# Kernel tuning notes

Hardware: AMD Instinct MI355X
Metric: run time of the kernel (lower is better)

## Reference

```python
import jax, jax.numpy as jnp
import numpy as np

N_NODES = 100000
N_EDGES = 1600000
IN_CH = 256
HID_CH = 32
OUT_CH = 8
N_GRAPHS = 64


def gcn_conv(x, edge_index, W, b):
    # PyG GCNConv: linear transform, add self-loops, symmetric norm, scatter-add.
    xw = x @ W  # [N, C_out]
    src, dst = edge_index[0], edge_index[1]
    loop = jnp.arange(N_NODES, dtype=src.dtype)
    src_f = jnp.concatenate([src, loop])  # [E+N]
    dst_f = jnp.concatenate([dst, loop])
    # degree over targets including self-loops (edge weight 1)
    deg = jax.ops.segment_sum(jnp.ones_like(dst_f, dtype=xw.dtype), dst_f,
                              num_segments=N_NODES)
    dinv = jnp.where(deg > 0, jax.lax.rsqrt(deg), 0.0)
    norm = dinv[src_f] * dinv[dst_f]  # [E+N]
    msgs = xw[src_f] * norm[:, None]  # gather + scale
    out = jax.ops.segment_sum(msgs, dst_f, num_segments=N_NODES)
    return out + b


def setup_inputs() -> dict:
    key = jax.random.key(0)
    k1, k2, k3, k4, k5, k6 = jax.random.split(key, 6)
    x = jax.random.normal(k1, (N_NODES, IN_CH), dtype=jnp.float32)
    edge_index = jax.random.randint(k2, (2, N_EDGES), 0, N_NODES, dtype=jnp.int64)
    batch = jnp.sort(jax.random.randint(k3, (N_NODES,), 0, N_GRAPHS, dtype=jnp.int64))
    s1 = 1.0 / np.sqrt(IN_CH)
    s2 = 1.0 / np.sqrt(HID_CH)
    W1 = jax.random.uniform(k4, (IN_CH, HID_CH), jnp.float32, -s1, s1)
    b1 = jnp.zeros((HID_CH,), jnp.float32)
    W2 = jax.random.uniform(k5, (HID_CH, OUT_CH), jnp.float32, -s2, s2)
    b2 = jnp.zeros((OUT_CH,), jnp.float32)
    return {"x": x, "edge_index": edge_index, "batch": batch,
            "W1": W1, "b1": b1, "W2": W2, "b2": b2}


def reference(x, edge_index, batch, W1, b1, W2, b2):
    h = jax.nn.relu(gcn_conv(x, edge_index, W1, b1))   # [N, HID]
    h = jax.nn.relu(gcn_conv(h, edge_index, W2, b2))   # [N, OUT]
    # global mean pool per graph
    sums = jax.ops.segment_sum(h, batch, num_segments=N_GRAPHS)
    cnts = jax.ops.segment_sum(jnp.ones((h.shape[0],), h.dtype), batch,
                               num_segments=N_GRAPHS)
    pooled = sums / jnp.maximum(cnts, 1.0)[:, None]    # [G, OUT]
    return jax.nn.log_softmax(pooled, axis=1)
```

## Files before the change

### kernel.cpp

```cpp
#include <hip/hip_runtime.h>
#include <hip/hip_bf16.h>
#include <math.h>

#define N_NODES 100000
#define N_EDGES 1600000
#define IN_CH 256
#define HID_CH 32
#define OUT_CH 8
#define N_GRAPHS 64

#define BUCK_SHIFT 7
#define NODES_PER_BUCK 128
#define NBUCK ((N_NODES + NODES_PER_BUCK - 1) / NODES_PER_BUCK)
#define CAP 2560
#define PCAP 3456
#define CHUNK 2048
#define NBLK_P1 ((N_EDGES + CHUNK - 1) / CHUNK)
#define ARENA (NBUCK * CAP)

#define DUMMY_ROW N_NODES
#define Y_ROWS 100008

#define OFF_DEG    0
#define OFF_DINV   (OFF_DEG + N_NODES)
#define OFF_ROWS   (OFF_DINV + N_NODES)
#define OFF_CNTG   (OFF_ROWS + N_NODES)
#define OFF_CSR    (OFF_CNTG + 784)
#define OFF_Y1     (OFF_CSR + NBUCK*PCAP)
#define OFF_BBUF   (OFF_Y1 + Y_ROWS*16)
#define OFF_Y2     (OFF_BBUF + ARENA)
#define OFF_PSUM   (OFF_Y2 + Y_ROWS*4)
#define OFF_PCNT   (OFF_PSUM + N_GRAPHS*OUT_CH)
#define OFF_WFRAG  (OFF_PCNT + 128)

typedef __attribute__((ext_vector_type(8))) short bf16x8;
typedef __attribute__((ext_vector_type(4))) float f32x4;

__device__ __forceinline__ unsigned bfr(float f) {
    unsigned u = __float_as_uint(f);
    return (u + 0x7fffu + ((u >> 16) & 1u)) >> 16;
}
__device__ __forceinline__ float bf_lo(unsigned w) { return __uint_as_float(w << 16); }
__device__ __forceinline__ float bf_hi(unsigned w) { return __uint_as_float(w & 0xffff0000u); }

#define ACC8(r) do { \
    a0 += bf_lo((r).x); a1 += bf_hi((r).x); a2 += bf_lo((r).y); a3 += bf_hi((r).y); \
    a4 += bf_lo((r).z); a5 += bf_hi((r).z); a6 += bf_lo((r).w); a7 += bf_hi((r).w); } while (0)

__global__ __launch_bounds__(256) void wprep_kernel(
        const float* __restrict__ W1, uint4* __restrict__ wfrag,
        unsigned* __restrict__ cntg, unsigned* __restrict__ y1w,
        unsigned* __restrict__ y2w) {
    const int t = threadIdx.x;
    if (blockIdx.x == 0) {
        for (int i = t; i < NBUCK; i += 256) cntg[i] = 0u;
        if (t < 16) y1w[(size_t)DUMMY_ROW * 16 + t] = 0u;
        if (t < 4)  y2w[(size_t)DUMMY_ROW * 4 + t] = 0u;
    }
    const int fl = blockIdx.x * 256 + t;
    const int f = fl >> 6, lane = fl & 63;
    const int kb = f >> 1, cb = f & 1;
    const int lr = lane & 15, lg = lane >> 4;
    unsigned short s[8];
#pragma unroll
    for (int j = 0; j < 8; j++)
        s[j] = (unsigned short)bfr(W1[(kb * 32 + lg * 8 + j) * 32 + cb * 16 + lr]);
    uint4 pk;
    pk.x = s[0] | ((unsigned)s[1] << 16);
    pk.y = s[2] | ((unsigned)s[3] << 16);
    pk.z = s[4] | ((unsigned)s[5] << 16);
    pk.w = s[6] | ((unsigned)s[7] << 16);
    wfrag[fl] = pk;
}

__global__ __launch_bounds__(256) void p1_partition(
        const int* __restrict__ src, const int* __restrict__ dst,
        unsigned* __restrict__ cntg, unsigned* __restrict__ bbuf) {
    __shared__ unsigned hcnt[NBUCK];
    __shared__ unsigned hcur[NBUCK];
    const int t = threadIdx.x;
    const long long e0 = (long long)blockIdx.x * CHUNK;

    int rs[8]; unsigned rd[8];
#pragma unroll
    for (int i = 0; i < 8; i++) {
        const long long e = e0 + t + i * 256;
        const bool v = (e < N_EDGES);
        rs[i] = v ? src[e] : 0;
        rd[i] = v ? (unsigned)dst[e] : 0xFFFFFFFFu;
    }
    for (int i = t; i < NBUCK; i += 256) hcnt[i] = 0;
    __syncthreads();
#pragma unroll
    for (int i = 0; i < 8; i++)
        if (rd[i] != 0xFFFFFFFFu) atomicAdd(&hcnt[rd[i] >> BUCK_SHIFT], 1u);
    __syncthreads();
    for (int i = t; i < NBUCK; i += 256) {
        const unsigned c = hcnt[i];
        const unsigned r = c ? atomicAdd(&cntg[i], c) : 0u;
        hcur[i] = (unsigned)i * CAP + r;
    }
    __syncthreads();
#pragma unroll
    for (int i = 0; i < 8; i++) {
        if (rd[i] != 0xFFFFFFFFu) {
            const unsigned b = rd[i] >> BUCK_SHIFT;
            const unsigned pos = atomicAdd(&hcur[b], 1u);
            if (pos - b * CAP < CAP)
                bbuf[pos] = (unsigned)rs[i] | ((rd[i] & (NODES_PER_BUCK - 1)) << 17);
        }
    }
}

__global__ __launch_bounds__(256) void p2_build(
        const unsigned* __restrict__ cntg,
        const unsigned* __restrict__ bbuf, int* __restrict__ csr,
        unsigned* __restrict__ deg, unsigned* __restrict__ rowstart,
        float* __restrict__ dinv) {
    __shared__ unsigned hist[NODES_PER_BUCK];
    __shared__ unsigned start[NODES_PER_BUCK];
    __shared__ unsigned cur[NODES_PER_BUCK];
    __shared__ unsigned s[256];
    __shared__ int lcsr[PCAP];
    const int b = blockIdx.x;
    const int t = threadIdx.x;
    unsigned cnt = cntg[b]; if (cnt > CAP) cnt = CAP;
    const unsigned* mybuf = bbuf + (size_t)b * CAP;

    if (t < NODES_PER_BUCK) hist[t] = 0;
    __syncthreads();
    for (unsigned i = t; i < cnt; i += 256) atomicAdd(&hist[mybuf[i] >> 17], 1u);
    __syncthreads();
    const unsigned d = (t < NODES_PER_BUCK) ? hist[t] : 0u;
    const unsigned pd = (d + 7u) & ~7u;
    s[t] = pd;
    __syncthreads();
    for (int off = 1; off < 256; off <<= 1) {
        unsigned x = (t >= off) ? s[t - off] : 0u;
        __syncthreads();
        s[t] += x;
        __syncthreads();
    }
    const unsigned total = s[255];
    const unsigned ex = s[t] - pd;
    if (t < NODES_PER_BUCK) { start[t] = ex; cur[t] = ex; }
    __syncthreads();
    for (unsigned i = t; i < total; i += 256) lcsr[i] = DUMMY_ROW;
    __syncthreads();
    for (unsigned i = t; i < cnt; i += 256) {
        const unsigned p = mybuf[i];
        const unsigned pos = atomicAdd(&cur[p >> 17], 1u);
        lcsr[pos] = (int)(p & 0x1FFFFu);
    }
    __syncthreads();
    const unsigned gbase = (unsigned)b * PCAP;
    for (unsigned i = t; i < total; i += 256) csr[gbase + i] = lcsr[i];
    const int n = b * NODES_PER_BUCK + t;
    if (t < NODES_PER_BUCK && n < N_NODES) {
        deg[n] = d;
        rowstart[n] = gbase + start[t];
        dinv[n] = rsqrtf((float)d + 1.0f);
    }
}

__global__ __launch_bounds__(256) void gemm1_kernel(
        const float* __restrict__ x, const uint4* __restrict__ wfrag,
        const float* __restrict__ dinv, unsigned short* __restrict__ y1bf,
        float* __restrict__ psum) {
    const int t = threadIdx.x;
    if (blockIdx.x == 0) {
        for (int i = t; i < N_GRAPHS * OUT_CH + N_GRAPHS; i += 256) psum[i] = 0.0f;
    }
    const int w = t >> 6;
    const int lane = t & 63;
    const int tile = blockIdx.x * 4 + w;
    if (tile >= N_NODES / 16) return;
    const int node0 = tile * 16;
    const int lr = lane & 15;
    const int lg = lane >> 4;

    bf16x8 bw[8][2];
#pragma unroll
    for (int kb = 0; kb < 8; kb++) {
#pragma unroll
        for (int cb = 0; cb < 2; cb++) {
            const uint4 v = wfrag[(kb * 2 + cb) * 64 + lane];
            bw[kb][cb] = *(const bf16x8*)&v;
        }
    }

    const float4* xr = (const float4*)(x + (size_t)(node0 + lr) * IN_CH);
    f32x4 acc0 = {0.f, 0.f, 0.f, 0.f}, acc1 = {0.f, 0.f, 0.f, 0.f};
#pragma unroll
    for (int kb = 0; kb < 8; kb++) {
        const float4 A = xr[kb * 8 + lg * 2];
        const float4 B = xr[kb * 8 + lg * 2 + 1];
        bf16x8 a;
        a[0] = (short)bfr(A.x); a[1] = (short)bfr(A.y);
        a[2] = (short)bfr(A.z); a[3] = (short)bfr(A.w);
        a[4] = (short)bfr(B.x); a[5] = (short)bfr(B.y);
        a[6] = (short)bfr(B.z); a[7] = (short)bfr(B.w);
        acc0 = __builtin_amdgcn_mfma_f32_16x16x32_bf16(a, bw[kb][0], acc0, 0, 0, 0);
        acc1 = __builtin_amdgcn_mfma_f32_16x16x32_bf16(a, bw[kb][1], acc1, 0, 0, 0);
    }

#pragma unroll
    for (int r = 0; r < 4; r++) {
        const int n = node0 + lg * 4 + r;
        const float dv = dinv[n];
        y1bf[(size_t)n * 32 + lr]      = (unsigned short)bfr(acc0[r] * dv);
        y1bf[(size_t)n * 32 + 16 + lr] = (unsigned short)bfr(acc1[r] * dv);
    }
}

__global__ __launch_bounds__(256) void g32l2_kernel(
        const unsigned* __restrict__ rowstart, const unsigned* __restrict__ deg,
        const int* __restrict__ csr, const uint4* __restrict__ y1v4,
        const float* __restrict__ dinv, const float* __restrict__ b1,
        const float* __restrict__ W2, uint4* __restrict__ y2v4) {
    __shared__ float w2s[HID_CH][9];
    __shared__ float b1s[HID_CH];
    const int t = threadIdx.x;
    { const int k = t >> 3, c = t & 7; w2s[k][c] = W2[t]; }
    if (t < HID_CH) b1s[t] = b1[t];
    __syncthreads();

    const int nl = t >> 2;
    const int q = t & 3;
    const int node = blockIdx.x * 64 + nl;
    if (node >= N_NODES) return;
    const int b4 = (t & 63) & ~3;

    const unsigned d = deg[node];
    const unsigned pd = (d + 7u) & ~7u;
    const unsigned base = rowstart[node];

    float a0, a1, a2, a3, a4, a5, a6, a7;
    { const uint4 sv = y1v4[(size_t)node * 4 + q];
      a0 = bf_lo(sv.x); a1 = bf_hi(sv.x); a2 = bf_lo(sv.y); a3 = bf_hi(sv.y);
      a4 = bf_lo(sv.z); a5 = bf_hi(sv.z); a6 = bf_lo(sv.w); a7 = bf_hi(sv.w); }

    unsigned j = 0;
    for (; j + 16 <= pd; j += 16) {
        const int4 e4 = ((const int4*)(csr + base + j))[q];
        const int s0  = __shfl(e4.x, b4 + 0);
        const int s1  = __shfl(e4.y, b4 + 0);
        const int s2  = __shfl(e4.z, b4 + 0);
        const int s3  = __shfl(e4.w, b4 + 0);
        const int s4  = __shfl(e4.x, b4 + 1);
        const int s5  = __shfl(e4.y, b4 + 1);
        const int s6  = __shfl(e4.z, b4 + 1);
        const int s7  = __shfl(e4.w, b4 + 1);
        const int s8  = __shfl(e4.x, b4 + 2);
        const int s9  = __shfl(e4.y, b4 + 2);
        const int s10 = __shfl(e4.z, b4 + 2);
        const int s11 = __shfl(e4.w, b4 + 2);
        const int s12 = __shfl(e4.x, b4 + 3);
        const int s13 = __shfl(e4.y, b4 + 3);
        const int s14 = __shfl(e4.z, b4 + 3);
        const int s15 = __shfl(e4.w, b4 + 3);
        const uint4 r0  = y1v4[(size_t)s0 * 4 + q];
        const uint4 r1  = y1v4[(size_t)s1 * 4 + q];
        const uint4 r2  = y1v4[(size_t)s2 * 4 + q];
        const uint4 r3  = y1v4[(size_t)s3 * 4 + q];
        const uint4 r4  = y1v4[(size_t)s4 * 4 + q];
        const uint4 r5  = y1v4[(size_t)s5 * 4 + q];
        const uint4 r6  = y1v4[(size_t)s6 * 4 + q];
        const uint4 r7  = y1v4[(size_t)s7 * 4 + q];
        const uint4 r8  = y1v4[(size_t)s8 * 4 + q];
        const uint4 r9  = y1v4[(size_t)s9 * 4 + q];
        const uint4 r10 = y1v4[(size_t)s10 * 4 + q];
        const uint4 r11 = y1v4[(size_t)s11 * 4 + q];
        const uint4 r12 = y1v4[(size_t)s12 * 4 + q];
        const uint4 r13 = y1v4[(size_t)s13 * 4 + q];
        const uint4 r14 = y1v4[(size_t)s14 * 4 + q];
        const uint4 r15 = y1v4[(size_t)s15 * 4 + q];
        ACC8(r0);  ACC8(r1);  ACC8(r2);  ACC8(r3);
        ACC8(r4);  ACC8(r5);  ACC8(r6);  ACC8(r7);
        ACC8(r8);  ACC8(r9);  ACC8(r10); ACC8(r11);
        ACC8(r12); ACC8(r13); ACC8(r14); ACC8(r15);
    }
    if (j < pd) {
        const int4 e4 = ((const int4*)(csr + base + j))[q & 1];
        const int s0 = __shfl(e4.x, b4);
        const int s1 = __shfl(e4.y, b4);
        const int s2 = __shfl(e4.z, b4);
        const int s3 = __shfl(e4.w, b4);
        const int s4 = __shfl(e4.x, b4 + 1);
        const int s5 = __shfl(e4.y, b4 + 1);
        const int s6 = __shfl(e4.z, b4 + 1);
        const int s7 = __shfl(e4.w, b4 + 1);
        const uint4 r0 = y1v4[(size_t)s0 * 4 + q];
        const uint4 r1 = y1v4[(size_t)s1 * 4 + q];
        const uint4 r2 = y1v4[(size_t)s2 * 4 + q];
        const uint4 r3 = y1v4[(size_t)s3 * 4 + q];
        const uint4 r4 = y1v4[(size_t)s4 * 4 + q];
        const uint4 r5 = y1v4[(size_t)s5 * 4 + q];
        const uint4 r6 = y1v4[(size_t)s6 * 4 + q];
        const uint4 r7 = y1v4[(size_t)s7 * 4 + q];
        ACC8(r0); ACC8(r1); ACC8(r2); ACC8(r3);
        ACC8(r4); ACC8(r5); ACC8(r6); ACC8(r7);
    }

    const float dv = dinv[node];
    float h[8];
    h[0] = fmaxf(fmaf(a0, dv, b1s[8 * q + 0]), 0.0f);
    h[1] = fmaxf(fmaf(a1, dv, b1s[8 * q + 1]), 0.0f);
    h[2] = fmaxf(fmaf(a2, dv, b1s[8 * q + 2]), 0.0f);
    h[3] = fmaxf(fmaf(a3, dv, b1s[8 * q + 3]), 0.0f);
    h[4] = fmaxf(fmaf(a4, dv, b1s[8 * q + 4]), 0.0f);
    h[5] = fmaxf(fmaf(a5, dv, b1s[8 * q + 5]), 0.0f);
    h[6] = fmaxf(fmaf(a6, dv, b1s[8 * q + 6]), 0.0f);
    h[7] = fmaxf(fmaf(a7, dv, b1s[8 * q + 7]), 0.0f);

    float p[8] = {0, 0, 0, 0, 0, 0, 0, 0};
#pragma unroll
    for (int i = 0; i < 8; i++) {
        const float hi = h[i];
#pragma unroll
        for (int c = 0; c < 8; c++) p[c] = fmaf(hi, w2s[8 * q + i][c], p[c]);
    }
#pragma unroll
    for (int c = 0; c < 8; c++) p[c] += __shfl_xor(p[c], 1);
#pragma unroll
    for (int c = 0; c < 8; c++) p[c] += __shfl_xor(p[c], 2);

    if (q == 0) {
        uint4 pk;
        pk.x = bfr(p[0] * dv) | (bfr(p[1] * dv) << 16);
        pk.y = bfr(p[2] * dv) | (bfr(p[3] * dv) << 16);
        pk.z = bfr(p[4] * dv) | (bfr(p[5] * dv) << 16);
        pk.w = bfr(p[6] * dv) | (bfr(p[7] * dv) << 16);
        y2v4[node] = pk;
    }
}

__global__ __launch_bounds__(256) void g8pool_kernel(
        const unsigned* __restrict__ rowstart, const unsigned* __restrict__ deg,
        const int* __restrict__ csr, const uint4* __restrict__ y2v4,
        const float* __restrict__ dinv, const float* __restrict__ b2,
        const int* __restrict__ batch,
        float* __restrict__ psum, float* __restrict__ pcnt) {
    __shared__ float ls[N_GRAPHS * OUT_CH];
    __shared__ float lc[N_GRAPHS];
    __shared__ float b2s[OUT_CH];
    __shared__ int grange[2];
    __shared__ float tr[32][8][9];
    const int t = threadIdx.x;
    ls[t] = 0.0f; ls[t + 256] = 0.0f;
    if (t < N_GRAPHS) lc[t] = 0.0f;
    if (t < OUT_CH) b2s[t] = b2[t];
    if (t == 0) { grange[0] = N_GRAPHS; grange[1] = -1; }
    __syncthreads();

    const int nl = t >> 3;
    const int l = t & 7;
    const int node = blockIdx.x * 32 + nl;
    const int g = batch[node];
    const unsigned d = deg[node];
    const unsigned pd = (d + 7u) & ~7u;
    const unsigned base = rowstart[node];

    float a0 = 0, a1 = 0, a2 = 0, a3 = 0, a4 = 0, a5 = 0, a6 = 0, a7 = 0;
    if (l == 0) { const uint4 sv = y2v4[node]; ACC8(sv); }
    for (unsigned j = 0; j < pd; j += 8) {
        const int si = csr[base + j + l];
        const uint4 r = y2v4[si];
        ACC8(r);
    }
    tr[nl][l][0] = a0; tr[nl][l][1] = a1; tr[nl][l][2] = a2; tr[nl][l][3] = a3;
    tr[nl][l][4] = a4; tr[nl][l][5] = a5; tr[nl][l][6] = a6; tr[nl][l][7] = a7;
    __syncthreads();
    float sc = 0.0f;
#pragma unroll
    for (int i = 0; i < 8; i++) sc += tr[nl][i][l];

    const float o = fmaxf(fmaf(sc, dinv[node], b2s[l]), 0.0f);
    atomicAdd(&ls[g * OUT_CH + l], o);
    if (l == 0) {
        atomicAdd(&lc[g], 1.0f);
        atomicMin(&grange[0], g);
        atomicMax(&grange[1], g);
    }
    __syncthreads();
    const int g0 = grange[0], g1 = grange[1];
    const int nent = (g1 - g0 + 1) * OUT_CH;
    for (int i = t; i < nent; i += 256)
        atomicAdd(&psum[g0 * OUT_CH + i], ls[g0 * OUT_CH + i]);
    for (int i = t; i < g1 - g0 + 1; i += 256)
        atomicAdd(&pcnt[g0 + i], lc[g0 + i]);
}

__global__ void logsoftmax_kernel(const float* __restrict__ psum,
                                  const float* __restrict__ pcnt,
                                  float* __restrict__ out) {
    const int g = threadIdx.x;
    if (g >= N_GRAPHS) return;
    const float cnt = fmaxf(pcnt[g], 1.0f);
    float p[OUT_CH];
    float m = -INFINITY;
#pragma unroll
    for (int c = 0; c < OUT_CH; c++) {
        p[c] = psum[g * OUT_CH + c] / cnt;
        m = fmaxf(m, p[c]);
    }
    float s = 0.0f;
#pragma unroll
    for (int c = 0; c < OUT_CH; c++) s += expf(p[c] - m);
    const float lse = logf(s);
#pragma unroll
    for (int c = 0; c < OUT_CH; c++) out[g * OUT_CH + c] = p[c] - m - lse;
}

extern "C" void kernel_launch(void* const* d_in, const int* in_sizes, int n_in,
                              void* d_out, int out_size, void* d_ws, size_t ws_size,
                              hipStream_t stream) {
    const float* x    = (const float*)d_in[0];
    const int* eidx   = (const int*)d_in[1];
    const int* batch  = (const int*)d_in[2];
    const float* W1   = (const float*)d_in[3];
    const float* b1   = (const float*)d_in[4];
    const float* W2   = (const float*)d_in[5];
    const float* b2   = (const float*)d_in[6];
    float* out = (float*)d_out;

    const int* src = eidx;
    const int* dst = eidx + N_EDGES;

    char* wsb = (char*)d_ws;
    unsigned* deg   = (unsigned*)(wsb) + OFF_DEG;
    float*    dinv  = (float*)(wsb) + OFF_DINV;
    unsigned* rows  = (unsigned*)(wsb) + OFF_ROWS;
    unsigned* cntg  = (unsigned*)(wsb) + OFF_CNTG;
    int*      csr   = (int*)(wsb) + OFF_CSR;
    unsigned* y1w   = (unsigned*)(wsb) + OFF_Y1;
    unsigned* bbuf  = (unsigned*)(wsb) + OFF_BBUF;
    unsigned* y2w   = (unsigned*)(wsb) + OFF_Y2;
    float*    psum  = (float*)(wsb) + OFF_PSUM;
    float*    pcnt  = (float*)(wsb) + OFF_PCNT;
    uint4*    wfrag = (uint4*)((unsigned*)(wsb) + OFF_WFRAG);

    wprep_kernel<<<4, 256, 0, stream>>>(W1, wfrag, cntg, y1w, y2w);
    p1_partition<<<NBLK_P1, 256, 0, stream>>>(src, dst, cntg, bbuf);
    p2_build<<<NBUCK, 256, 0, stream>>>(cntg, bbuf, csr, deg, rows, dinv);
    gemm1_kernel<<<(N_NODES / 16 + 3) / 4, 256, 0, stream>>>(
        x, wfrag, dinv, (unsigned short*)y1w, psum);
    g32l2_kernel<<<(N_NODES + 63) / 64, 256, 0, stream>>>(rows, deg, csr, (const uint4*)y1w,
                                                          dinv, b1, W2, (uint4*)y2w);
    g8pool_kernel<<<N_NODES / 32, 256, 0, stream>>>(rows, deg, csr, (const uint4*)y2w,
                                                    dinv, b2, batch, psum, pcnt);
    logsoftmax_kernel<<<1, 64, 0, stream>>>(psum, pcnt, out);
}
```

Measured before the change: 128.5 us.

## Merge CSR build with GEMM1, apply source norm at gather, fuse log-softmax

The CSR build and the first GEMM now run in one launch, with block index choosing the role, so the GEMM no longer waits for dinv. Because of that, the source-side dinv scaling moves out of the GEMM epilogue and into the layer-1 gather, which loads dinv per neighbor (dummy rows padded with zeros). The layer-2 pooling replaces its shared-memory transpose reduction with wave shuffles and unrolls its loop two-wide. A last-block ticket folds the log-softmax into the pool kernel, removing one launch. The cost is an extra dinv gather per edge and an atomic ticket with a fence.

Result: slower. 303.8 us (+136.4%).

```diff
diff --git a/kernel.cpp b/kernel.cpp
--- a/kernel.cpp
+++ b/kernel.cpp
@@ -21,9 +21,13 @@
 #define DUMMY_ROW N_NODES
 #define Y_ROWS 100008
 
+#define GEMM_TILES (N_NODES / 16)
+#define GEMM_BLKS ((GEMM_TILES + 3) / 4)
+#define POOL_BLKS (N_NODES / 32)
+
 #define OFF_DEG    0
 #define OFF_DINV   (OFF_DEG + N_NODES)
-#define OFF_ROWS   (OFF_DINV + N_NODES)
+#define OFF_ROWS   (OFF_DINV + N_NODES + 8)
 #define OFF_CNTG   (OFF_ROWS + N_NODES)
 #define OFF_CSR    (OFF_CNTG + 784)
 #define OFF_Y1     (OFF_CSR + NBUCK*PCAP)
@@ -31,7 +35,8 @@
 #define OFF_Y2     (OFF_BBUF + ARENA)
 #define OFF_PSUM   (OFF_Y2 + Y_ROWS*4)
 #define OFF_PCNT   (OFF_PSUM + N_GRAPHS*OUT_CH)
-#define OFF_WFRAG  (OFF_PCNT + 128)
+#define OFF_DONE   (OFF_PCNT + 64)
+#define OFF_WFRAG  (OFF_DONE + 64)
 
 typedef __attribute__((ext_vector_type(8))) short bf16x8;
 typedef __attribute__((ext_vector_type(4))) float f32x4;
@@ -47,15 +52,25 @@
     a0 += bf_lo((r).x); a1 += bf_hi((r).x); a2 += bf_lo((r).y); a3 += bf_hi((r).y); \
     a4 += bf_lo((r).z); a5 += bf_hi((r).z); a6 += bf_lo((r).w); a7 += bf_hi((r).w); } while (0)
 
+#define ACC8S(r, dv) do { \
+    a0 = fmaf(bf_lo((r).x), (dv), a0); a1 = fmaf(bf_hi((r).x), (dv), a1); \
+    a2 = fmaf(bf_lo((r).y), (dv), a2); a3 = fmaf(bf_hi((r).y), (dv), a3); \
+    a4 = fmaf(bf_lo((r).z), (dv), a4); a5 = fmaf(bf_hi((r).z), (dv), a5); \
+    a6 = fmaf(bf_lo((r).w), (dv), a6); a7 = fmaf(bf_hi((r).w), (dv), a7); } while (0)
+
 __global__ __launch_bounds__(256) void wprep_kernel(
         const float* __restrict__ W1, uint4* __restrict__ wfrag,
         unsigned* __restrict__ cntg, unsigned* __restrict__ y1w,
-        unsigned* __restrict__ y2w) {
+        unsigned* __restrict__ y2w, float* __restrict__ psum,
+        float* __restrict__ dinv, unsigned* __restrict__ done) {
     const int t = threadIdx.x;
     if (blockIdx.x == 0) {
         for (int i = t; i < NBUCK; i += 256) cntg[i] = 0u;
+        for (int i = t; i < N_GRAPHS * OUT_CH + N_GRAPHS; i += 256) psum[i] = 0.0f;
         if (t < 16) y1w[(size_t)DUMMY_ROW * 16 + t] = 0u;
         if (t < 4)  y2w[(size_t)DUMMY_ROW * 4 + t] = 0u;
+        if (t < 8)  dinv[DUMMY_ROW + t] = 0.0f;
+        if (t == 0) done[0] = 0u;
     }
     const int fl = blockIdx.x * 256 + t;
     const int f = fl >> 6, lane = fl & 63;
@@ -112,104 +127,98 @@
     }
 }
 
-__global__ __launch_bounds__(256) void p2_build(
-        const unsigned* __restrict__ cntg,
-        const unsigned* __restrict__ bbuf, int* __restrict__ csr,
-        unsigned* __restrict__ deg, unsigned* __restrict__ rowstart,
-        float* __restrict__ dinv) {
+__global__ __launch_bounds__(256) void p2g1_kernel(
+        const unsigned* __restrict__ cntg, const unsigned* __restrict__ bbuf,
+        int* __restrict__ csr, unsigned* __restrict__ deg,
+        unsigned* __restrict__ rowstart, float* __restrict__ dinv,
+        const float* __restrict__ x, const uint4* __restrict__ wfrag,
+        unsigned short* __restrict__ y1bf) {
     __shared__ unsigned hist[NODES_PER_BUCK];
     __shared__ unsigned start[NODES_PER_BUCK];
     __shared__ unsigned cur[NODES_PER_BUCK];
     __shared__ unsigned s[256];
     __shared__ int lcsr[PCAP];
-    const int b = blockIdx.x;
     const int t = threadIdx.x;
-    unsigned cnt = cntg[b]; if (cnt > CAP) cnt = CAP;
-    const unsigned* mybuf = bbuf + (size_t)b * CAP;
-
-    if (t < NODES_PER_BUCK) hist[t] = 0;
-    __syncthreads();
-    for (unsigned i = t; i < cnt; i += 256) atomicAdd(&hist[mybuf[i] >> 17], 1u);
-    __syncthreads();
-    const unsigned d = (t < NODES_PER_BUCK) ? hist[t] : 0u;
-    const unsigned pd = (d + 7u) & ~7u;
-    s[t] = pd;
-    __syncthreads();
-    for (int off = 1; off < 256; off <<= 1) {
-        unsigned x = (t >= off) ? s[t - off] : 0u;
-        __syncthreads();
-        s[t] += x;
-        __syncthreads();
-    }
-    const unsigned total = s[255];
-    const unsigned ex = s[t] - pd;
-    if (t < NODES_PER_BUCK) { start[t] = ex; cur[t] = ex; }
-    __syncthreads();
-    for (unsigned i = t; i < total; i += 256) lcsr[i] = DUMMY_ROW;
-    __syncthreads();
-    for (unsigned i = t; i < cnt; i += 256) {
-        const unsigned p = mybuf[i];
-        const unsigned pos = atomicAdd(&cur[p >> 17], 1u);
-        lcsr[pos] = (int)(p & 0x1FFFFu);
-    }
-    __syncthreads();
-    const unsigned gbase = (unsigned)b * PCAP;
-    for (unsigned i = t; i < total; i += 256) csr[gbase + i] = lcsr[i];
-    const int n = b * NODES_PER_BUCK + t;
-    if (t < NODES_PER_BUCK && n < N_NODES) {
-        deg[n] = d;
-        rowstart[n] = gbase + start[t];
-        dinv[n] = rsqrtf((float)d + 1.0f);
-    }
-}
-
-__global__ __launch_bounds__(256) void gemm1_kernel(
-        const float* __restrict__ x, const uint4* __restrict__ wfrag,
-        const float* __restrict__ dinv, unsigned short* __restrict__ y1bf,
-        float* __restrict__ psum) {
-    const int t = threadIdx.x;
-    if (blockIdx.x == 0) {
-        for (int i = t; i < N_GRAPHS * OUT_CH + N_GRAPHS; i += 256) psum[i] = 0.0f;
-    }
-    const int w = t >> 6;
-    const int lane = t & 63;
-    const int tile = blockIdx.x * 4 + w;
-    if (tile >= N_NODES / 16) return;
-    const int node0 = tile * 16;
-    const int lr = lane & 15;
-    const int lg = lane >> 4;
-
-    bf16x8 bw[8][2];
-#pragma unroll
-    for (int kb = 0; kb < 8; kb++) {
-#pragma unroll
-        for (int cb = 0; cb < 2; cb++) {
-            const uint4 v = wfrag[(kb * 2 + cb) * 64 + lane];
-            bw[kb][cb] = *(const bf16x8*)&v;
-        }
-    }
-
-    const float4* xr = (const float4*)(x + (size_t)(node0 + lr) * IN_CH);
-    f32x4 acc0 = {0.f, 0.f, 0.f, 0.f}, acc1 = {0.f, 0.f, 0.f, 0.f};
-#pragma unroll
-    for (int kb = 0; kb < 8; kb++) {
-        const float4 A = xr[kb * 8 + lg * 2];
-        const float4 B = xr[kb * 8 + lg * 2 + 1];
-        bf16x8 a;
-        a[0] = (short)bfr(A.x); a[1] = (short)bfr(A.y);
-        a[2] = (short)bfr(A.z); a[3] = (short)bfr(A.w);
-        a[4] = (short)bfr(B.x); a[5] = (short)bfr(B.y);
-        a[6] = (short)bfr(B.z); a[7] = (short)bfr(B.w);
-        acc0 = __builtin_amdgcn_mfma_f32_16x16x32_bf16(a, bw[kb][0], acc0, 0, 0, 0);
-        acc1 = __builtin_amdgcn_mfma_f32_16x16x32_bf16(a, bw[kb][1], acc1, 0, 0, 0);
-    }
-
-#pragma unroll
-    for (int r = 0; r < 4; r++) {
-        const int n = node0 + lg * 4 + r;
-        const float dv = dinv[n];
-        y1bf[(size_t)n * 32 + lr]      = (unsigned short)bfr(acc0[r] * dv);
-        y1bf[(size_t)n * 32 + 16 + lr] = (unsigned short)bfr(acc1[r] * dv);
+
+    if (blockIdx.x < NBUCK) {
+        const int b = blockIdx.x;
+        unsigned cnt = cntg[b]; if (cnt > CAP) cnt = CAP;
+        const unsigned* mybuf = bbuf + (size_t)b * CAP;
+
+        if (t < NODES_PER_BUCK) hist[t] = 0;
+        __syncthreads();
+        for (unsigned i = t; i < cnt; i += 256) atomicAdd(&hist[mybuf[i] >> 17], 1u);
+        __syncthreads();
+        const unsigned d = (t < NODES_PER_BUCK) ? hist[t] : 0u;
+        const unsigned pd = (d + 7u) & ~7u;
+        s[t] = pd;
+        __syncthreads();
+        for (int off = 1; off < 256; off <<= 1) {
+            unsigned xv = (t >= off) ? s[t - off] : 0u;
+            __syncthreads();
+            s[t] += xv;
+            __syncthreads();
+        }
+        const unsigned total = s[255];
+        const unsigned ex = s[t] - pd;
+        if (t < NODES_PER_BUCK) { start[t] = ex; cur[t] = ex; }
+        __syncthreads();
+        for (unsigned i = t; i < total; i += 256) lcsr[i] = DUMMY_ROW;
+        __syncthreads();
+        for (unsigned i = t; i < cnt; i += 256) {
+            const unsigned p = mybuf[i];
+            const unsigned pos = atomicAdd(&cur[p >> 17], 1u);
+            lcsr[pos] = (int)(p & 0x1FFFFu);
+        }
+        __syncthreads();
+        const unsigned gbase = (unsigned)b * PCAP;
+        for (unsigned i = t; i < total; i += 256) csr[gbase + i] = lcsr[i];
+        const int n = b * NODES_PER_BUCK + t;
+        if (t < NODES_PER_BUCK && n < N_NODES) {
+            deg[n] = d;
+            rowstart[n] = gbase + start[t];
+            dinv[n] = rsqrtf((float)d + 1.0f);
+        }
+    } else {
+        const int w = t >> 6;
+        const int lane = t & 63;
+        const int tile = (blockIdx.x - NBUCK) * 4 + w;
+        if (tile >= GEMM_TILES) return;
+        const int node0 = tile * 16;
+        const int lr = lane & 15;
+        const int lg = lane >> 4;
+
+        bf16x8 bw[8][2];
+#pragma unroll
+        for (int kb = 0; kb < 8; kb++) {
+#pragma unroll
+            for (int cb = 0; cb < 2; cb++) {
+                const uint4 v = wfrag[(kb * 2 + cb) * 64 + lane];
+                bw[kb][cb] = *(const bf16x8*)&v;
+            }
+        }
+
+        const float4* xr = (const float4*)(x + (size_t)(node0 + lr) * IN_CH);
+        f32x4 acc0 = {0.f, 0.f, 0.f, 0.f}, acc1 = {0.f, 0.f, 0.f, 0.f};
+#pragma unroll
+        for (int kb = 0; kb < 8; kb++) {
+            const float4 A = xr[kb * 8 + lg * 2];
+            const float4 B = xr[kb * 8 + lg * 2 + 1];
+            bf16x8 a;
+            a[0] = (short)bfr(A.x); a[1] = (short)bfr(A.y);
+            a[2] = (short)bfr(A.z); a[3] = (short)bfr(A.w);
+            a[4] = (short)bfr(B.x); a[5] = (short)bfr(B.y);
+            a[6] = (short)bfr(B.z); a[7] = (short)bfr(B.w);
+            acc0 = __builtin_amdgcn_mfma_f32_16x16x32_bf16(a, bw[kb][0], acc0, 0, 0, 0);
+            acc1 = __builtin_amdgcn_mfma_f32_16x16x32_bf16(a, bw[kb][1], acc1, 0, 0, 0);
+        }
+
+#pragma unroll
+        for (int r = 0; r < 4; r++) {
+            const int n = node0 + lg * 4 + r;
+            y1bf[(size_t)n * 32 + lr]      = (unsigned short)bfr(acc0[r]);
+            y1bf[(size_t)n * 32 + 16 + lr] = (unsigned short)bfr(acc1[r]);
+        }
     }
 }
 
@@ -234,31 +243,34 @@
     const unsigned d = deg[node];
     const unsigned pd = (d + 7u) & ~7u;
     const unsigned base = rowstart[node];
-
-    float a0, a1, a2, a3, a4, a5, a6, a7;
-    { const uint4 sv = y1v4[(size_t)node * 4 + q];
-      a0 = bf_lo(sv.x); a1 = bf_hi(sv.x); a2 = bf_lo(sv.y); a3 = bf_hi(sv.y);
-      a4 = bf_lo(sv.z); a5 = bf_hi(sv.z); a6 = bf_lo(sv.w); a7 = bf_hi(sv.w); }
+    const float dvn = dinv[node];
+
+    float a0 = 0, a1 = 0, a2 = 0, a3 = 0, a4 = 0, a5 = 0, a6 = 0, a7 = 0;
+    { const uint4 sv = y1v4[(size_t)node * 4 + q]; ACC8S(sv, dvn); }
 
     unsigned j = 0;
     for (; j + 16 <= pd; j += 16) {
         const int4 e4 = ((const int4*)(csr + base + j))[q];
-        const int s0  = __shfl(e4.x, b4 + 0);
-        const int s1  = __shfl(e4.y, b4 + 0);
-        const int s2  = __shfl(e4.z, b4 + 0);
-        const int s3  = __shfl(e4.w, b4 + 0);
-        const int s4  = __shfl(e4.x, b4 + 1);
-        const int s5  = __shfl(e4.y, b4 + 1);
-        const int s6  = __shfl(e4.z, b4 + 1);
-        const int s7  = __shfl(e4.w, b4 + 1);
-        const int s8  = __shfl(e4.x, b4 + 2);
-        const int s9  = __shfl(e4.y, b4 + 2);
-        const int s10 = __shfl(e4.z, b4 + 2);
-        const int s11 = __shfl(e4.w, b4 + 2);
-        const int s12 = __shfl(e4.x, b4 + 3);
-        const int s13 = __shfl(e4.y, b4 + 3);
-        const int s14 = __shfl(e4.z, b4 + 3);
-        const int s15 = __shfl(e4.w, b4 + 3);
+        const float da = dinv[e4.x];
+        const float db = dinv[e4.y];
+        const float dc = dinv[e4.z];
+        const float dd = dinv[e4.w];
+        const int s0  = __shfl(e4.x, b4 + 0); const float v0  = __shfl(da, b4 + 0);
+        const int s1  = __shfl(e4.y, b4 + 0); const float v1  = __shfl(db, b4 + 0);
+        const int s2  = __shfl(e4.z, b4 + 0); const float v2  = __shfl(dc, b4 + 0);
+        const int s3  = __shfl(e4.w, b4 + 0); const float v3  = __shfl(dd, b4 + 0);
+        const int s4  = __shfl(e4.x, b4 + 1); const float v4  = __shfl(da, b4 + 1);
+        const int s5  = __shfl(e4.y, b4 + 1); const float v5  = __shfl(db, b4 + 1);
+        const int s6  = __shfl(e4.z, b4 + 1); const float v6  = __shfl(dc, b4 + 1);
+        const int s7  = __shfl(e4.w, b4 + 1); const float v7  = __shfl(dd, b4 + 1);
+        const int s8  = __shfl(e4.x, b4 + 2); const float v8  = __shfl(da, b4 + 2);
+        const int s9  = __shfl(e4.y, b4 + 2); const float v9  = __shfl(db, b4 + 2);
+        const int s10 = __shfl(e4.z, b4 + 2); const float v10 = __shfl(dc, b4 + 2);
+        const int s11 = __shfl(e4.w, b4 + 2); const float v11 = __shfl(dd, b4 + 2);
+        const int s12 = __shfl(e4.x, b4 + 3); const float v12 = __shfl(da, b4 + 3);
+        const int s13 = __shfl(e4.y, b4 + 3); const float v13 = __shfl(db, b4 + 3);
+        const int s14 = __shfl(e4.z, b4 + 3); const float v14 = __shfl(dc, b4 + 3);
+        const int s15 = __shfl(e4.w, b4 + 3); const float v15 = __shfl(dd, b4 + 3);
         const uint4 r0  = y1v4[(size_t)s0 * 4 + q];
         const uint4 r1  = y1v4[(size_t)s1 * 4 + q];
         const uint4 r2  = y1v4[(size_t)s2 * 4 + q];
@@ -275,21 +287,25 @@
         const uint4 r13 = y1v4[(size_t)s13 * 4 + q];
         const uint4 r14 = y1v4[(size_t)s14 * 4 + q];
         const uint4 r15 = y1v4[(size_t)s15 * 4 + q];
-        ACC8(r0);  ACC8(r1);  ACC8(r2);  ACC8(r3);
-        ACC8(r4);  ACC8(r5);  ACC8(r6);  ACC8(r7);
-        ACC8(r8);  ACC8(r9);  ACC8(r10); ACC8(r11);
-        ACC8(r12); ACC8(r13); ACC8(r14); ACC8(r15);
+        ACC8S(r0, v0);   ACC8S(r1, v1);   ACC8S(r2, v2);   ACC8S(r3, v3);
+        ACC8S(r4, v4);   ACC8S(r5, v5);   ACC8S(r6, v6);   ACC8S(r7, v7);
+        ACC8S(r8, v8);   ACC8S(r9, v9);   ACC8S(r10, v10); ACC8S(r11, v11);
+        ACC8S(r12, v12); ACC8S(r13, v13); ACC8S(r14, v14); ACC8S(r15, v15);
     }
     if (j < pd) {
         const int4 e4 = ((const int4*)(csr + base + j))[q & 1];
-        const int s0 = __shfl(e4.x, b4);
-        const int s1 = __shfl(e4.y, b4);
-        const int s2 = __shfl(e4.z, b4);
-        const int s3 = __shfl(e4.w, b4);
-        const int s4 = __shfl(e4.x, b4 + 1);
-        const int s5 = __shfl(e4.y, b4 + 1);
-        const int s6 = __shfl(e4.z, b4 + 1);
-        const int s7 = __shfl(e4.w, b4 + 1);
+        const float da = dinv[e4.x];
+        const float db = dinv[e4.y];
+        const float dc = dinv[e4.z];
+        const float dd = dinv[e4.w];
+        const int s0 = __shfl(e4.x, b4);     const float v0 = __shfl(da, b4);
+        const int s1 = __shfl(e4.y, b4);     const float v1 = __shfl(db, b4);
+        const int s2 = __shfl(e4.z, b4);     const float v2 = __shfl(dc, b4);
+        const int s3 = __shfl(e4.w, b4);     const float v3 = __shfl(dd, b4);
+        const int s4 = __shfl(e4.x, b4 + 1); const float v4 = __shfl(da, b4 + 1);
+        const int s5 = __shfl(e4.y, b4 + 1); const float v5 = __shfl(db, b4 + 1);
+        const int s6 = __shfl(e4.z, b4 + 1); const float v6 = __shfl(dc, b4 + 1);
+        const int s7 = __shfl(e4.w, b4 + 1); const float v7 = __shfl(dd, b4 + 1);
         const uint4 r0 = y1v4[(size_t)s0 * 4 + q];
         const uint4 r1 = y1v4[(size_t)s1 * 4 + q];
         const uint4 r2 = y1v4[(size_t)s2 * 4 + q];
@@ -298,20 +314,19 @@
         const uint4 r5 = y1v4[(size_t)s5 * 4 + q];
         const uint4 r6 = y1v4[(size_t)s6 * 4 + q];
         const uint4 r7 = y1v4[(size_t)s7 * 4 + q];
-        ACC8(r0); ACC8(r1); ACC8(r2); ACC8(r3);
-        ACC8(r4); ACC8(r5); ACC8(r6); ACC8(r7);
-    }
-
-    const float dv = dinv[node];
+        ACC8S(r0, v0); ACC8S(r1, v1); ACC8S(r2, v2); ACC8S(r3, v3);
+        ACC8S(r4, v4); ACC8S(r5, v5); ACC8S(r6, v6); ACC8S(r7, v7);
+    }
+
     float h[8];
-    h[0] = fmaxf(fmaf(a0, dv, b1s[8 * q + 0]), 0.0f);
-    h[1] = fmaxf(fmaf(a1, dv, b1s[8 * q + 1]), 0.0f);
-    h[2] = fmaxf(fmaf(a2, dv, b1s[8 * q + 2]), 0.0f);
-    h[3] = fmaxf(fmaf(a3, dv, b1s[8 * q + 3]), 0.0f);
-    h[4] = fmaxf(fmaf(a4, dv, b1s[8 * q + 4]), 0.0f);
-    h[5] = fmaxf(fmaf(a5, dv, b1s[8 * q + 5]), 0.0f);
-    h[6] = fmaxf(fmaf(a6, dv, b1s[8 * q + 6]), 0.0f);
-    h[7] = fmaxf(fmaf(a7, dv, b1s[8 * q + 7]), 0.0f);
+    h[0] = fmaxf(fmaf(a0, dvn, b1s[8 * q + 0]), 0.0f);
+    h[1] = fmaxf(fmaf(a1, dvn, b1s[8 * q + 1]), 0.0f);
+    h[2] = fmaxf(fmaf(a2, dvn, b1s[8 * q + 2]), 0.0f);
+    h[3] = fmaxf(fmaf(a3, dvn, b1s[8 * q + 3]), 0.0f);
+    h[4] = fmaxf(fmaf(a4, dvn, b1s[8 * q + 4]), 0.0f);
+    h[5] = fmaxf(fmaf(a5, dvn, b1s[8 * q + 5]), 0.0f);
+    h[6] = fmaxf(fmaf(a6, dvn, b1s[8 * q + 6]), 0.0f);
+    h[7] = fmaxf(fmaf(a7, dvn, b1s[8 * q + 7]), 0.0f);
 
     float p[8] = {0, 0, 0, 0, 0, 0, 0, 0};
 #pragma unroll
@@ -327,10 +342,10 @@
 
     if (q == 0) {
         uint4 pk;
-        pk.x = bfr(p[0] * dv) | (bfr(p[1] * dv) << 16);
-        pk.y = bfr(p[2] * dv) | (bfr(p[3] * dv) << 16);
-        pk.z = bfr(p[4] * dv) | (bfr(p[5] * dv) << 16);
-        pk.w = bfr(p[6] * dv) | (bfr(p[7] * dv) << 16);
+        pk.x = bfr(p[0] * dvn) | (bfr(p[1] * dvn) << 16);
+        pk.y = bfr(p[2] * dvn) | (bfr(p[3] * dvn) << 16);
+        pk.z = bfr(p[4] * dvn) | (bfr(p[5] * dvn) << 16);
+        pk.w = bfr(p[6] * dvn) | (bfr(p[7] * dvn) << 16);
         y2v4[node] = pk;
     }
 }
@@ -340,12 +355,13 @@
         const int* __restrict__ csr, const uint4* __restrict__ y2v4,
         const float* __restrict__ dinv, const float* __restrict__ b2,
         const int* __restrict__ batch,
-        float* __restrict__ psum, float* __restrict__ pcnt) {
+        float* __restrict__ psum, float* __restrict__ pcnt,
+        unsigned* __restrict__ done, float* __restrict__ out) {
     __shared__ float ls[N_GRAPHS * OUT_CH];
     __shared__ float lc[N_GRAPHS];
     __shared__ float b2s[OUT_CH];
     __shared__ int grange[2];
-    __shared__ float tr[32][8][9];
+    __shared__ unsigned ticket_s;
     const int t = threadIdx.x;
     ls[t] = 0.0f; ls[t + 256] = 0.0f;
     if (t < N_GRAPHS) lc[t] = 0.0f;
@@ -363,17 +379,30 @@
 
     float a0 = 0, a1 = 0, a2 = 0, a3 = 0, a4 = 0, a5 = 0, a6 = 0, a7 = 0;
     if (l == 0) { const uint4 sv = y2v4[node]; ACC8(sv); }
-    for (unsigned j = 0; j < pd; j += 8) {
-        const int si = csr[base + j + l];
-        const uint4 r = y2v4[si];
-        ACC8(r);
-    }
-    tr[nl][l][0] = a0; tr[nl][l][1] = a1; tr[nl][l][2] = a2; tr[nl][l][3] = a3;
-    tr[nl][l][4] = a4; tr[nl][l][5] = a5; tr[nl][l][6] = a6; tr[nl][l][7] = a7;
-    __syncthreads();
-    float sc = 0.0f;
-#pragma unroll
-    for (int i = 0; i < 8; i++) sc += tr[nl][i][l];
+    unsigned j = 0;
+    for (; j + 16 <= pd; j += 16) {
+        const int sa = csr[base + j + l];
+        const int sb = csr[base + j + 8 + l];
+        const uint4 ra = y2v4[sa];
+        const uint4 rb = y2v4[sb];
+        ACC8(ra); ACC8(rb);
+    }
+    if (j < pd) {
+        const int sa = csr[base + j + l];
+        const uint4 ra = y2v4[sa];
+        ACC8(ra);
+    }
+    a0 += __shfl_xor(a0, 1); a1 += __shfl_xor(a1, 1); a2 += __shfl_xor(a2, 1);
+    a3 += __shfl_xor(a3, 1); a4 += __shfl_xor(a4, 1); a5 += __shfl_xor(a5, 1);
+    a6 += __shfl_xor(a6, 1); a7 += __shfl_xor(a7, 1);
+    a0 += __shfl_xor(a0, 2); a1 += __shfl_xor(a1, 2); a2 += __shfl_xor(a2, 2);
+    a3 += __shfl_xor(a3, 2); a4 += __shfl_xor(a4, 2); a5 += __shfl_xor(a5, 2);
+    a6 += __shfl_xor(a6, 2); a7 += __shfl_xor(a7, 2);
+    a0 += __shfl_xor(a0, 4); a1 += __shfl_xor(a1, 4); a2 += __shfl_xor(a2, 4);
+    a3 += __shfl_xor(a3, 4); a4 += __shfl_xor(a4, 4); a5 += __shfl_xor(a5, 4);
+    a6 += __shfl_xor(a6, 4); a7 += __shfl_xor(a7, 4);
+    const float sc = (l < 4) ? ((l < 2) ? (l == 0 ? a0 : a1) : (l == 2 ? a2 : a3))
+                             : ((l < 6) ? (l == 4 ? a4 : a5) : (l == 6 ? a6 : a7));
 
     const float o = fmaxf(fmaf(sc, dinv[node], b2s[l]), 0.0f);
     atomicAdd(&ls[g * OUT_CH + l], o);
@@ -389,27 +418,27 @@
         atomicAdd(&psum[g0 * OUT_CH + i], ls[g0 * OUT_CH + i]);
     for (int i = t; i < g1 - g0 + 1; i += 256)
         atomicAdd(&pcnt[g0 + i], lc[g0 + i]);
-}
-
-__global__ void logsoftmax_kernel(const float* __restrict__ psum,
-                                  const float* __restrict__ pcnt,
-                                  float* __restrict__ out) {
-    const int g = threadIdx.x;
-    if (g >= N_GRAPHS) return;
-    const float cnt = fmaxf(pcnt[g], 1.0f);
-    float p[OUT_CH];
-    float m = -INFINITY;
-#pragma unroll
-    for (int c = 0; c < OUT_CH; c++) {
-        p[c] = psum[g * OUT_CH + c] / cnt;
-        m = fmaxf(m, p[c]);
-    }
-    float s = 0.0f;
-#pragma unroll
-    for (int c = 0; c < OUT_CH; c++) s += expf(p[c] - m);
-    const float lse = logf(s);
-#pragma unroll
-    for (int c = 0; c < OUT_CH; c++) out[g * OUT_CH + c] = p[c] - m - lse;
+
+    __threadfence();
+    __syncthreads();
+    if (t == 0) ticket_s = atomicAdd(done, 1u);
+    __syncthreads();
+    if (ticket_s == POOL_BLKS - 1 && t < N_GRAPHS) {
+        const float cnt = fmaxf(atomicAdd(&pcnt[t], 0.0f), 1.0f);
+        float p[OUT_CH];
+        float m = -INFINITY;
+#pragma unroll
+        for (int c = 0; c < OUT_CH; c++) {
+            p[c] = atomicAdd(&psum[t * OUT_CH + c], 0.0f) / cnt;
+            m = fmaxf(m, p[c]);
+        }
+        float ssum = 0.0f;
+#pragma unroll
+        for (int c = 0; c < OUT_CH; c++) ssum += expf(p[c] - m);
+        const float lse = logf(ssum);
+#pragma unroll
+        for (int c = 0; c < OUT_CH; c++) out[t * OUT_CH + c] = p[c] - m - lse;
+    }
 }
 
 extern "C" void kernel_launch(void* const* d_in, const int* in_sizes, int n_in,
@@ -438,16 +467,15 @@
     unsigned* y2w   = (unsigned*)(wsb) + OFF_Y2;
     float*    psum  = (float*)(wsb) + OFF_PSUM;
     float*    pcnt  = (float*)(wsb) + OFF_PCNT;
+    unsigned* done  = (unsigned*)(wsb) + OFF_DONE;
     uint4*    wfrag = (uint4*)((unsigned*)(wsb) + OFF_WFRAG);
 
-    wprep_kernel<<<4, 256, 0, stream>>>(W1, wfrag, cntg, y1w, y2w);
+    wprep_kernel<<<4, 256, 0, stream>>>(W1, wfrag, cntg, y1w, y2w, psum, dinv, done);
     p1_partition<<<NBLK_P1, 256, 0, stream>>>(src, dst, cntg, bbuf);
-    p2_build<<<NBUCK, 256, 0, stream>>>(cntg, bbuf, csr, deg, rows, dinv);
-    gemm1_kernel<<<(N_NODES / 16 + 3) / 4, 256, 0, stream>>>(
-        x, wfrag, dinv, (unsigned short*)y1w, psum);
+    p2g1_kernel<<<NBUCK + GEMM_BLKS, 256, 0, stream>>>(
+        cntg, bbuf, csr, deg, rows, dinv, x, wfrag, (unsigned short*)y1w);
     g32l2_kernel<<<(N_NODES + 63) / 64, 256, 0, stream>>>(rows, deg, csr, (const uint4*)y1w,
                                                           dinv, b1, W2, (uint4*)y2w);
-    g8pool_kernel<<<N_NODES / 32, 256, 0, stream>>>(rows, deg, csr, (const uint4*)y2w,
-                                                    dinv, b2, batch, psum, pcnt);
-    logsoftmax_kernel<<<1, 64, 0, stream>>>(psum, pcnt, out);
-}
+    g8pool_kernel<<<POOL_BLKS, 256, 0, stream>>>(rows, deg, csr, (const uint4*)y2w,
+                                                 dinv, b2, batch, psum, pcnt, done, out);
+}
```
